# Performance work log

Hardware: AMD Instinct MI355X
Metric: run time of the kernel (lower is better)

The kernel has to match this reference:

```python
import jax, jax.numpy as jnp
import numpy as np


def _gru_step(x, h, W_ih, W_hh, b_ih, b_hh):
    # torch GRUCell math, gate order (r, z, n)
    gx = x @ W_ih.T + b_ih
    gh = h @ W_hh.T + b_hh
    xr, xz, xn = jnp.split(gx, 3, axis=-1)
    hr, hz, hn = jnp.split(gh, 3, axis=-1)
    r = jax.nn.sigmoid(xr + hr)
    z = jax.nn.sigmoid(xz + hz)
    n = jnp.tanh(xn + r * hn)
    return (1.0 - z) * n + z * h


def setup_inputs() -> dict:
    T, B, S, E, H, Dv, EXT = 64, 16, 400, 128, 256, 50000, 50
    key = jax.random.key(0)
    ks = jax.random.split(key, 32)
    def rn(k, shape, s=0.05):
        return jax.random.normal(k, shape, dtype=jnp.float32) * s
    return {
        'embedded_y': rn(ks[0], (T, B, E), 1.0),
        'encode_outputs': rn(ks[1], (S, B, 2 * H), 1.0),
        'init_state': rn(ks[2], (B, H), 1.0),
        'x_mask': jnp.ones((S, B, 1), jnp.float32),
        'y_mask': jnp.ones((T, B, 1), jnp.float32),
        'x_index': jax.random.randint(ks[3], (S, B), 0, Dv + EXT),
        'max_ext_len': EXT,
        'init_coverage': jnp.zeros((B, S), jnp.float32),
        'W_h': rn(ks[4], (2 * H, 2 * H)),
        'W_s': rn(ks[5], (2 * H, H)),
        'W_c': rn(ks[6], (2 * H, 1)),
        'b_attn': rn(ks[7], (2 * H,)),
        'V_attn': rn(ks[8], (1, 2 * H)),
        'gru1_Wih': rn(ks[9], (3 * H, E)),
        'gru1_Whh': rn(ks[10], (3 * H, H)),
        'gru1_bih': rn(ks[11], (3 * H,)),
        'gru1_bhh': rn(ks[12], (3 * H,)),
        'gru2_Wih': rn(ks[13], (3 * H, 2 * H)),
        'gru2_Whh': rn(ks[14], (3 * H, H)),
        'gru2_bih': rn(ks[15], (3 * H,)),
        'gru2_bhh': rn(ks[16], (3 * H,)),
        'V1_w': rn(ks[17], (H, H + 2 * H + E)),
        'V1_b': rn(ks[18], (H,)),
        'V2_w': rn(ks[19], (Dv, H)),
        'V2_b': rn(ks[20], (Dv,)),
        'Wp_w': rn(ks[21], (1, H + 2 * H + E)),
        'Wp_b': rn(ks[22], (1,)),
    }


def reference(embedded_y, encode_outputs, init_state, x_mask, y_mask, x_index,
              max_ext_len, init_coverage, W_h, W_s, W_c, b_attn, V_attn,
              gru1_Wih, gru1_Whh, gru1_bih, gru1_bhh,
              gru2_Wih, gru2_Whh, gru2_bih, gru2_bhh,
              V1_w, V1_b, V2_w, V2_b, Wp_w, Wp_b):
    T, B, E = embedded_y.shape
    S = encode_outputs.shape[0]
    enc_proj = encode_outputs @ W_h.T  # [S,B,2H], time-invariant part of attention

    def step(carry, inp):
        hidden, cov = carry  # [B,H], [B,S]
        y_t, ym_t = inp      # [B,E], [B,1]
        s1 = _gru_step(y_t, hidden, gru1_Wih, gru1_Whh, gru1_bih, gru1_bhh)
        s1 = ym_t * s1 + (1.0 - ym_t) * hidden
        # coverage term: cov.T[:,:,None] is [S,B,1], Linear(1,2H)
        att = enc_proj + s1 @ W_s.T + cov.T[:, :, None] @ W_c.T + b_attn  # [S,B,2H]
        score = (jnp.tanh(att) * x_mask) @ V_attn.T                      # [S,B,1]
        score = jnp.where(x_mask == 0, -1e9, score)
        attn = jax.nn.softmax(score, axis=0)                             # over source len
        ctx = jnp.sum(attn * encode_outputs, axis=0)                     # [B,2H]
        s2 = _gru_step(ctx, s1, gru2_Wih, gru2_Whh, gru2_bih, gru2_bhh)
        s2 = ym_t * s2 + (1.0 - ym_t) * s1
        waw = attn[:, :, 0].T                                            # [B,S]
        return (s2, cov + waw), (s2, ctx, waw, cov)

    (_, _), (hs, cvs, waws, covs) = jax.lax.scan(
        step, (init_state, init_coverage), (embedded_y, y_mask))

    # WordProbLayer (pointer-generator)
    h = jnp.concatenate([hs, cvs, embedded_y], axis=2)         # [T,B,H+2H+E]
    logit = jnp.tanh(h @ V1_w.T + V1_b) @ V2_w.T + V2_b        # [T,B,Dv]
    y_dec = jax.nn.softmax(logit, axis=2)
    y_dec = jnp.concatenate(
        [y_dec, jnp.zeros((T, B, max_ext_len), y_dec.dtype)], axis=2)
    g = jax.nn.sigmoid(h @ Wp_w.T + Wp_b)                      # [T,B,1]
    xids = jnp.broadcast_to(x_index.T[None], (T, B, S))        # [T,B,S]
    ti = jnp.arange(T)[:, None, None]
    bi = jnp.arange(B)[None, :, None]
    y_pred = (g * y_dec).at[ti, bi, xids].add((1.0 - g) * waws)
    return (y_pred, hs, waws, covs)
```

## Files before the change

kernel.cpp:

```cpp
#include <hip/hip_runtime.h>
#include <hip/hip_bf16.h>

typedef unsigned short ushort_t;
typedef unsigned int u32;
typedef _Float16 f16;
typedef __attribute__((ext_vector_type(8))) short short8;
typedef __attribute__((ext_vector_type(4))) float f32x4;
typedef __attribute__((ext_vector_type(8))) _Float16 f16x8;
typedef __attribute__((ext_vector_type(4))) unsigned int u32x4;

#define T_ 64
#define B_ 16
#define S_ 400
#define E_ 128
#define H_ 256
#define H2_ 512
#define DV_ 50000
#define VOC_ 50050
#define CAT_ 896
#define NCLUS 8
#define RSL 50

#define YP_SZ   ((size_t)T_*B_*VOC_)
#define HS_OFF  (YP_SZ)
#define WW_OFF  (HS_OFF + (size_t)T_*B_*H_)
#define CV_OFF  (WW_OFF + (size_t)T_*B_*S_)
#define ENCP16_OFF ((size_t)0)
#define ENC16_OFF  ((size_t)1638400)
#define WS16_OFF   ((size_t)3276800)
#define W216_OFF   ((size_t)3342336)
#define CTXALL_OFF ((size_t)3538944)
#define GX1_OFF    ((size_t)4063232)
#define WH216_OFF  ((size_t)4947968)
#define WH116T_OFF ((size_t)5046272)
#define SYNC_OFF   ((size_t)5144576)
#define S1STR      528
#define S1TAG      520
#define S2STR      816
#define S2TAG      808
#define S2REG      ((size_t)16*NCLUS*S1STR)
#define SYNC_FLOATS ((size_t)16*NCLUS*(S1STR + S2STR))
#define WH16F_OFF  ((size_t)5316608)
#define V1HF_OFF   ((size_t)5447680)

#define WS_ROWSUM 0
#define WS_GV     1024
#define WS_G1     2048

__device__ __forceinline__ float fsig(float x){ return 1.f/(1.f+__expf(-x)); }
__device__ __forceinline__ float ftanh(float x){ float e=__expf(2.f*x); return 1.f - 2.f/(e+1.f); }

#define PADK(k) ((k) + (((k)>>5)<<2))

#define AT_ST(p, v)  __hip_atomic_store((p), (v), __ATOMIC_RELAXED, __HIP_MEMORY_SCOPE_AGENT)
#define AT_LD(p)     __hip_atomic_load((p), __ATOMIC_RELAXED, __HIP_MEMORY_SCOPE_AGENT)
#define AT_STI(p, v) __hip_atomic_store((int*)(p), (v), __ATOMIC_RELAXED, __HIP_MEMORY_SCOPE_AGENT)
#define AT_LDI(p)    __hip_atomic_load((const int*)(p), __ATOMIC_RELAXED, __HIP_MEMORY_SCOPE_AGENT)

#define SM_ENC    0
#define SM_ENCP   51200
#define SM_GH1    102400
#define SM_SWS    105472
#define SM_VP     107776
#define SM_WCP    110080
#define SM_UCTX   112384
#define SM_HID    114432
#define SM_S1     115456
#define SM_G2X    116480
#define SM_G2H    116864
#define SM_COV    117248
#define SM_EV     117504
#define SM_XM     117760
#define SM_YM     118016
#define SM_HIDH   118272
#define SM_S1H    118784
#define SM_CTXH   119296
#define SM_S2S    120320
#define SM_PART   120448
#define SM_B1     120512
#define SM_B2     123584
#define SM_B3     126656
#define SM_GX     129728
#define SM_BYTES  132800

__global__ __launch_bounds__(256)
void cvt16_kernel(const float* src, f16* dst, int n){
  int i = blockIdx.x*256 + threadIdx.x;
  if (i < n) dst[i] = (f16)src[i];
}

__global__ __launch_bounds__(256)
void repack_kernel(const float* enc, f16* enc16){
  int s = blockIdx.x, b = blockIdx.y;
  const float* src = enc + ((size_t)s*B_ + b)*H2_;
  f16* dst = enc16 + ((size_t)b*S_ + s)*H2_;
  for (int k = threadIdx.x; k < H2_; k += 256) dst[k] = (f16)src[k];
}

__global__ __launch_bounds__(256)
void packWhh1_kernel(const float* W, f16* dst){
  int r = blockIdx.x, c = threadIdx.x;
  int jq = c >> 5, cc = c & 31;
  dst[((size_t)jq*768 + r)*32 + cc] = (f16)W[(size_t)r*H_ + c];
}

__global__ __launch_bounds__(256)
void gx1_kernel(const float* emb, const float* Wih1, const float* bih1, float* dout){
  __shared__ float As[64][33];
  __shared__ float Bs[128][33];
  int m0 = blockIdx.x*64, n0 = blockIdx.y*128;
  int tx = threadIdx.x & 15, ty = threadIdx.x >> 4;
  float acc[4][8] = {};
  for (int kt = 0; kt < E_; kt += 32){
    for (int l = threadIdx.x; l < 64*32; l += 256){
      int m = l>>5, k = l&31; As[m][k] = emb[(size_t)(m0+m)*E_ + kt + k];
    }
    for (int l = threadIdx.x; l < 128*32; l += 256){
      int n = l>>5, k = l&31; Bs[n][k] = Wih1[(size_t)(n0+n)*E_ + kt + k];
    }
    __syncthreads();
    for (int k = 0; k < 32; ++k){
      float a[4], bv[8];
      #pragma unroll
      for (int i=0;i<4;++i) a[i] = As[ty+16*i][k];
      #pragma unroll
      for (int j=0;j<8;++j) bv[j] = Bs[tx+16*j][k];
      #pragma unroll
      for (int i=0;i<4;++i)
        #pragma unroll
        for (int j=0;j<8;++j) acc[i][j] += a[i]*bv[j];
    }
    __syncthreads();
  }
  #pragma unroll
  for (int i=0;i<4;++i)
    #pragma unroll
    for (int j=0;j<8;++j){
      int m = m0 + ty + 16*i, n = n0 + tx + 16*j;
      dout[GX1_OFF + (size_t)m*768 + n] = acc[i][j] + bih1[n];
    }
}

__global__ __launch_bounds__(256)
void encproj_mfma(const f16* enc16, const f16* Wh16, const float* battn, f16* ep16){
  int nx = blockIdx.x, my = blockIdx.y, bz = blockIdx.z;
  int tid = threadIdx.x;
  int w = tid >> 6, lane = tid & 63;
  int c16 = lane & 15, kg = lane >> 4;
  int m0 = my*64, n0 = nx*128 + w*32;
  f32x4 acc[4][2] = {};
  int col0 = n0 + c16, col1 = n0 + 16 + c16;
  for (int ks = 0; ks < 16; ++ks){
    int k0 = ks*32 + kg*8;
    f16x8 b0 = *(const f16x8*)(Wh16 + (size_t)col0*H2_ + k0);
    f16x8 b1 = *(const f16x8*)(Wh16 + (size_t)col1*H2_ + k0);
    #pragma unroll
    for (int mf = 0; mf < 4; ++mf){
      int s = m0 + mf*16 + c16; if (s > S_-1) s = S_-1;
      f16x8 a = *(const f16x8*)(enc16 + ((size_t)bz*S_ + s)*H2_ + k0);
      acc[mf][0] = __builtin_amdgcn_mfma_f32_16x16x32_f16(a, b0, acc[mf][0], 0, 0, 0);
      acc[mf][1] = __builtin_amdgcn_mfma_f32_16x16x32_f16(a, b1, acc[mf][1], 0, 0, 0);
    }
  }
  #pragma unroll
  for (int mf = 0; mf < 4; ++mf)
    #pragma unroll
    for (int nf = 0; nf < 2; ++nf){
      int col = n0 + nf*16 + c16;
      float bb = battn[col];
      #pragma unroll
      for (int r = 0; r < 4; ++r){
        int s = m0 + mf*16 + kg*4 + r;
        if (s < S_) ep16[((size_t)bz*S_ + s)*H2_ + col] = (f16)(acc[mf][nf][r] + bb);
      }
    }
}

template<int R, int K, bool PAD>
__device__ __forceinline__ void gemv_f16t(const f16* W, const f16* xh, float* out_l, int tid){
  int o = tid >> 3, l8 = tid & 7;
  constexpr int NI = K/64;
  const f16x8* x8 = (const f16x8*)xh;
  f16x8 xv[NI];
  #pragma unroll
  for (int i = 0; i < NI; ++i) xv[i] = x8[i*8 + l8];
  #pragma unroll
  for (int it = 0; it < R/128; ++it){
    int d = o + it*128;
    const f16x8* w8 = (const f16x8*)(W + (size_t)d*K);
    float acc = 0.f;
    #pragma unroll
    for (int i = 0; i < NI; ++i){
      f16x8 w = w8[i*8 + l8];
      #pragma unroll
      for (int e = 0; e < 8; ++e) acc += (float)w[e] * (float)xv[i][e];
    }
    acc += __shfl_xor(acc,1,8); acc += __shfl_xor(acc,2,8); acc += __shfl_xor(acc,4,8);
    if (l8 == 0) out_l[PAD ? PADK(d) : d] = acc;
  }
}

__device__ __forceinline__ void spin_tags(const float* base, int stride, int tagoff, int want, int tid){
  if (tid < 64){
    bool mine = tid < NCLUS;
    const float* tp = base + (size_t)(mine ? tid : 0)*stride + tagoff;
    while (true){
      int v = mine ? AT_LDI(tp) : want;
      if (__all(v == want)) break;
      __builtin_amdgcn_s_sleep(1);
    }
  }
  __syncthreads();
}

__global__ __launch_bounds__(1024)
void scan_kernel(const float* xm, const float* ym,
                 const float* bhh1, const float* bih2, const float* bhh2,
                 const float* Wc, const float* Vat,
                 const float* inith, const float* initc,
                 float* dout)
{
  extern __shared__ char smem[];
  f16*   enc_s  = (f16*)(smem + SM_ENC);
  f16*   encp_s = (f16*)(smem + SM_ENCP);
  float* gh1_l  = (float*)(smem + SM_GH1);
  float* sWs_p  = (float*)(smem + SM_SWS);
  float* Vp     = (float*)(smem + SM_VP);
  float* Wcp    = (float*)(smem + SM_WCP);
  float* uctx   = (float*)(smem + SM_UCTX);
  float* hid_l  = (float*)(smem + SM_HID);
  float* s1_l   = (float*)(smem + SM_S1);
  float* g2x_l  = (float*)(smem + SM_G2X);
  float* g2h_l  = (float*)(smem + SM_G2H);
  float* cov_l  = (float*)(smem + SM_COV);
  float* ev_l   = (float*)(smem + SM_EV);
  float* xm_l   = (float*)(smem + SM_XM);
  float* ym_l   = (float*)(smem + SM_YM);
  f16*   hidh   = (f16*)(smem + SM_HIDH);
  f16*   s1h    = (f16*)(smem + SM_S1H);
  f16*   ctxh   = (f16*)(smem + SM_CTXH);
  float* s2s    = (float*)(smem + SM_S2S);
  float* part_l = (float*)(smem + SM_PART);
  float* b1l    = (float*)(smem + SM_B1);
  float* b2l    = (float*)(smem + SM_B2);
  float* b3l    = (float*)(smem + SM_B3);
  float* gxbuf  = (float*)(smem + SM_GX);

  const f16* Ws16   = (const f16*)(dout + WS16_OFF);
  const f16* W216   = (const f16*)(dout + W216_OFF);
  const f16* Wh216  = (const f16*)(dout + WH216_OFF);
  const f16* Wh116T = (const f16*)(dout + WH116T_OFF);
  const float* gx1  = dout + GX1_OFF;

  int blk = blockIdx.x, tid = threadIdx.x;
  int b = blk & 15, jj = blk >> 4;
  int wv = tid >> 6, ln = tid & 63;

  float* sl1 = dout + SYNC_OFF + (size_t)b*NCLUS*S1STR;
  float* sl2 = dout + SYNC_OFF + S2REG + (size_t)b*NCLUS*S2STR;
  float* sl1my = sl1 + (size_t)jj*S1STR;
  float* sl2my = sl2 + (size_t)jj*S2STR;

  {
    const u32x4* encg  = (const u32x4*)(dout + ENC16_OFF)  + (size_t)b*25600 + jj*3200;
    const u32x4* encpg = (const u32x4*)(dout + ENCP16_OFF) + (size_t)b*25600 + jj*3200;
    u32x4* encs4  = (u32x4*)enc_s;
    u32x4* encps4 = (u32x4*)encp_s;
    for (int i = tid; i < 3200; i += 1024){ encs4[i] = encg[i]; encps4[i] = encpg[i]; }
  }
  if (tid < 32)  s2s[tid] = inith[b*H_ + jj*32 + tid];
  if (tid < 512){ Vp[PADK(tid)] = Vat[tid]; Wcp[PADK(tid)] = Wc[tid]; }
  if (tid < RSL){ int s = jj*RSL + tid; cov_l[tid] = initc[b*S_ + s]; xm_l[tid] = xm[(size_t)s*B_ + b]; }
  if (tid >= 512 && tid < 576) ym_l[tid-512] = ym[(tid-512)*B_ + b];
  if (tid < 768){ b1l[tid] = bhh1[tid]; b2l[tid] = bih2[tid]; b3l[tid] = bhh2[tid];
                  gxbuf[tid] = gx1[(size_t)b*768 + tid]; }
  __syncthreads();
  if (tid < 768){
    const f16x8* p8 = (const f16x8*)(Wh116T + ((size_t)jj*768 + tid)*32);
    float acc = 0.f;
    #pragma unroll
    for (int c4 = 0; c4 < 4; ++c4){
      f16x8 w = p8[c4];
      #pragma unroll
      for (int e = 0; e < 8; ++e) acc += (float)w[e] * s2s[c4*8+e];
    }
    AT_ST(&sl2my[tid], acc);
  } else if (tid < 800){
    AT_ST(&sl2my[768 + (tid-768)], s2s[tid-768]);
  }
  __syncthreads();
  if (tid == 0) AT_STI(&sl2my[S2TAG], 1);

  for (int t = 0; t < T_; ++t){
    int row = t*B_ + b;
    int want = t + 1;
    spin_tags(sl2, S2STR, S2TAG, want, tid);
    if (tid < 768){
      float a = 0.f;
      #pragma unroll
      for (int q = 0; q < NCLUS; ++q) a += AT_LD(&sl2[(size_t)q*S2STR + tid]);
      gh1_l[tid] = a;
    } else {
      int j = tid - 768;
      float h = AT_LD(&sl2[(size_t)(j>>5)*S2STR + 768 + (j&31)]);
      hid_l[j] = h; hidh[j] = (f16)h;
    }
    __syncthreads();
    if (tid < 256){
      int j = tid;
      float r = fsig(gxbuf[j]      + gh1_l[j]      + b1l[j]);
      float z = fsig(gxbuf[256+j]  + gh1_l[256+j]  + b1l[256+j]);
      float n = ftanh(gxbuf[512+j] + r*(gh1_l[512+j] + b1l[512+j]));
      float h = hid_l[j];
      float ymv = ym_l[t];
      float s1 = ymv*((1.f-z)*n + z*h) + (1.f-ymv)*h;
      s1_l[j] = s1; s1h[j] = (f16)s1;
    }
    __syncthreads();
    gemv_f16t<512,256,true>(Ws16, s1h, sWs_p, tid);
    __syncthreads();
    {
      int kp = PADK(ln*8);
      float4 sA = *(const float4*)&sWs_p[kp], sB = *(const float4*)&sWs_p[kp+4];
      float4 vA = *(const float4*)&Vp[kp],    vB = *(const float4*)&Vp[kp+4];
      float4 cA = *(const float4*)&Wcp[kp],   cB = *(const float4*)&Wcp[kp+4];
      const f16x8* eps = (const f16x8*)encp_s;
      #pragma unroll
      for (int i = 0; i < 4; ++i){
        int r = wv + 16*i;
        if (r < RSL){
          f16x8 eu = eps[r*64 + ln];
          float cv = cov_l[r];
          float sc = 0.f;
          sc += ftanh((float)eu[0] + sA.x + cv*cA.x)*vA.x;
          sc += ftanh((float)eu[1] + sA.y + cv*cA.y)*vA.y;
          sc += ftanh((float)eu[2] + sA.z + cv*cA.z)*vA.z;
          sc += ftanh((float)eu[3] + sA.w + cv*cA.w)*vA.w;
          sc += ftanh((float)eu[4] + sB.x + cv*cB.x)*vB.x;
          sc += ftanh((float)eu[5] + sB.y + cv*cB.y)*vB.y;
          sc += ftanh((float)eu[6] + sB.z + cv*cB.z)*vB.z;
          sc += ftanh((float)eu[7] + sB.w + cv*cB.w)*vB.w;
          sc += __shfl_xor(sc,1);  sc += __shfl_xor(sc,2);  sc += __shfl_xor(sc,4);
          sc += __shfl_xor(sc,8);  sc += __shfl_xor(sc,16); sc += __shfl_xor(sc,32);
          if (ln == 0){
            float xmv = xm_l[r];
            ev_l[r] = __expf((xmv == 0.f) ? -1e9f : xmv*sc);
          }
        }
      }
    }
    __syncthreads();
    if (tid < 512){
      float acc = 0.f;
      #pragma unroll 5
      for (int s = 0; s < RSL; ++s) acc += ev_l[s] * (float)enc_s[s*H2_ + tid];
      AT_ST(&sl1my[tid], acc);
    } else if (tid >= 960){
      int l = tid - 960;
      float v = (l < RSL) ? ev_l[l] : 0.f;
      v += __shfl_xor(v,1);  v += __shfl_xor(v,2);  v += __shfl_xor(v,4);
      v += __shfl_xor(v,8);  v += __shfl_xor(v,16); v += __shfl_xor(v,32);
      if (l == 0) AT_ST(&sl1my[512], v);
    }
    __syncthreads();
    if (tid == 0) AT_STI(&sl1my[S1TAG], want);
    float gxn = 0.f;
    if (tid < 768){
      int tn = (t+1 < T_) ? t+1 : t;
      gxn = gx1[(size_t)(tn*B_ + b)*768 + tid];
    }
    {
      int o = tid >> 3, l8 = tid & 7;
      if (o < 96){
        int g = o >> 5, m = o & 31, wrow = g*256 + jj*32 + m;
        const f16x8* w8 = (const f16x8*)(Wh216 + (size_t)wrow*H_);
        const f16x8* x8 = (const f16x8*)s1h;
        float acc = 0.f;
        #pragma unroll
        for (int i = 0; i < 4; ++i){
          f16x8 w = w8[i*8 + l8], x = x8[i*8 + l8];
          #pragma unroll
          for (int e = 0; e < 8; ++e) acc += (float)w[e] * (float)x[e];
        }
        acc += __shfl_xor(acc,1,8); acc += __shfl_xor(acc,2,8); acc += __shfl_xor(acc,4,8);
        if (l8 == 0) g2h_l[o] = acc;
      }
    }
    if (tid < 768) gxbuf[tid] = gxn;
    spin_tags(sl1, S1STR, S1TAG, want, tid);
    if (tid < 512){
      float us = 0.f;
      #pragma unroll
      for (int q = 0; q < NCLUS; ++q) us += AT_LD(&sl1[(size_t)q*S1STR + tid]);
      uctx[tid] = us;
    } else if (tid < 512 + NCLUS){
      part_l[tid-512] = AT_LD(&sl1[(size_t)(tid-512)*S1STR + 512]);
    }
    __syncthreads();
    {
      float es = 0.f;
      #pragma unroll
      for (int q = 0; q < NCLUS; ++q) es += part_l[q];
      float inv = 1.f/es;
      if (tid < 512){
        float v = uctx[tid]*inv;
        ctxh[tid] = (f16)v;
        if (jj == 0) __builtin_nontemporal_store(v, &dout[CTXALL_OFF + (size_t)row*H2_ + tid]);
      } else if (tid >= 640 && tid < 640 + RSL){
        int r = tid - 640;
        float w_ = ev_l[r]*inv;
        size_t ro = (size_t)row*S_ + jj*RSL + r;
        __builtin_nontemporal_store(w_, &dout[WW_OFF + ro]);
        float co = cov_l[r];
        __builtin_nontemporal_store(co, &dout[CV_OFF + ro]);
        cov_l[r] = co + w_;
      }
    }
    __syncthreads();
    {
      int o = tid >> 3, l8 = tid & 7;
      if (o < 96){
        int g = o >> 5, m = o & 31, wrow = g*256 + jj*32 + m;
        const f16x8* w8 = (const f16x8*)(W216 + (size_t)wrow*H2_);
        const f16x8* x8 = (const f16x8*)ctxh;
        float acc = 0.f;
        #pragma unroll
        for (int i = 0; i < 8; ++i){
          f16x8 w = w8[i*8 + l8], x = x8[i*8 + l8];
          #pragma unroll
          for (int e = 0; e < 8; ++e) acc += (float)w[e] * (float)x[e];
        }
        acc += __shfl_xor(acc,1,8); acc += __shfl_xor(acc,2,8); acc += __shfl_xor(acc,4,8);
        if (l8 == 0) g2x_l[o] = acc;
      }
    }
    __syncthreads();
    if (tid < 32){
      int i = tid, j = jj*32 + i;
      float r = fsig(g2x_l[i]     + b2l[j]     + g2h_l[i]    + b3l[j]);
      float z = fsig(g2x_l[32+i]  + b2l[256+j] + g2h_l[32+i] + b3l[256+j]);
      float n = ftanh(g2x_l[64+i] + b2l[512+j] + r*(g2h_l[64+i] + b3l[512+j]));
      float s1v = s1_l[j];
      float ymv = ym_l[t];
      float s2 = ymv*((1.f-z)*n + z*s1v) + (1.f-ymv)*s1v;
      s2s[i] = s2;
      AT_ST(&sl2my[768 + i], s2);
      __builtin_nontemporal_store(s2, &dout[HS_OFF + (size_t)row*H_ + j]);
    }
    __syncthreads();
    if (tid < 768){
      const f16x8* p8 = (const f16x8*)(Wh116T + ((size_t)jj*768 + tid)*32);
      float acc = 0.f;
      #pragma unroll
      for (int c4 = 0; c4 < 4; ++c4){
        f16x8 w = p8[c4];
        #pragma unroll
        for (int e = 0; e < 8; ++e) acc += (float)w[e] * s2s[c4*8+e];
      }
      AT_ST(&sl2my[tid], acc);
    }
    __syncthreads();
    if (tid == 0) AT_STI(&sl2my[S2TAG], t + 2);
  }
}

__global__ __launch_bounds__(512)
void head_kernel(const float* emb, const f16* V1H, const float* V1b,
                 const float* Wpw, const float* Wpb, float* dout, float* ws)
{
  __shared__ float hc[2][CAT_];
  int t = blockIdx.x, b0 = blockIdx.y*2, tid = threadIdx.x;
  for (int i = tid; i < 2*CAT_; i += 512){
    int bb = i / CAT_, k = i % CAT_;
    int b = b0 + bb;
    float v;
    if (k < H_)           v = dout[HS_OFF     + ((size_t)(t*B_+b))*H_  + k];
    else if (k < H_+H2_)  v = dout[CTXALL_OFF + ((size_t)(t*B_+b))*H2_ + (k-H_)];
    else                  v = emb[((size_t)(t*B_+b))*E_ + (k-H_-H2_)];
    hc[bb][k] = v;
  }
  __syncthreads();
  __hip_bfloat16* G1 = (__hip_bfloat16*)(ws + WS_G1);
  {
    int j = tid & 255, bb = tid >> 8;
    const f16x8* wv8 = (const f16x8*)(V1H + (size_t)j*CAT_);
    float acc = 0.f;
    #pragma unroll 4
    for (int kk = 0; kk < CAT_/8; ++kk){
      f16x8 w = wv8[kk];
      #pragma unroll
      for (int e = 0; e < 8; ++e) acc += hc[bb][kk*8+e]*(float)w[e];
    }
    G1[((size_t)(t*B_ + b0 + bb))*H_ + j] = __float2bfloat16(ftanh(acc + V1b[j]));
  }
  if (tid < 128){
    int bb = tid >> 6, l = tid & 63;
    float acc = 0.f;
    for (int k = l; k < CAT_; k += 64) acc += hc[bb][k]*Wpw[k];
    acc += __shfl_xor(acc,1);  acc += __shfl_xor(acc,2);  acc += __shfl_xor(acc,4);
    acc += __shfl_xor(acc,8);  acc += __shfl_xor(acc,16); acc += __shfl_xor(acc,32);
    if (l == 0) ws[WS_GV + t*B_ + b0 + bb] = fsig(acc + Wpb[0]);
  }
}

__global__ __launch_bounds__(256)
void gemm2_kernel(const ushort_t* G1, const float* V2w, const float* V2b,
                  float* dout, float* rowsum)
{
  __shared__ float rows_l[256];
  int tid = threadIdx.x;
  rows_l[tid] = 0.f;
  int m0 = blockIdx.y * 256;
  int n0 = blockIdx.x * 64;
  int lane = tid & 63, w = tid >> 6;
  int c16 = lane & 15, kg = lane >> 4;
  int col = n0 + w*16 + c16;
  int colc = col < DV_ ? col : DV_-1;
  bool valid = col < DV_;
  f32x4 acc[16] = {};
  const float* brow = V2w + (size_t)colc*H_;
  for (int ks = 0; ks < 8; ++ks){
    int k0 = ks*32 + kg*8;
    short8 bf;
    #pragma unroll
    for (int i = 0; i < 8; ++i){
      __hip_bfloat16 hb = __float2bfloat16(brow[k0+i]);
      union { __hip_bfloat16 h; short s; } u; u.h = hb;
      bf[i] = u.s;
    }
    #pragma unroll
    for (int mf = 0; mf < 16; ++mf){
      const short8* ap = (const short8*)(G1 + ((size_t)(m0 + mf*16 + c16))*H_ + k0);
      acc[mf] = __builtin_amdgcn_mfma_f32_16x16x32_bf16(*ap, bf, acc[mf], 0, 0, 0);
    }
  }
  float bias = valid ? V2b[colc] : 0.f;
  __syncthreads();
  #pragma unroll
  for (int mf = 0; mf < 16; ++mf){
    #pragma unroll
    for (int r = 0; r < 4; ++r){
      float v = valid ? __expf(acc[mf][r] + bias) : 0.f;
      int rloc = mf*16 + kg*4 + r;
      if (valid) __builtin_nontemporal_store(v, &dout[(size_t)(m0 + rloc)*VOC_ + col]);
      float s = v;
      s += __shfl_xor(s, 1, 16); s += __shfl_xor(s, 2, 16);
      s += __shfl_xor(s, 4, 16); s += __shfl_xor(s, 8, 16);
      if (c16 == 0) atomicAdd(&rows_l[rloc], s);
    }
  }
  __syncthreads();
  atomicAdd(&rowsum[m0 + tid], rows_l[tid]);
}

__global__ __launch_bounds__(256)
void normscatter_kernel(float* dout, const float* ws, const int* xidx){
  int row = blockIdx.x; int b = row & 15;
  float gv = ws[WS_GV + row];
  float sc = gv / ws[WS_ROWSUM + row];
  float g1 = 1.f - gv;
  float2* y2 = (float2*)(dout + (size_t)row * VOC_);
  for (int i = threadIdx.x; i < VOC_/2; i += 256){
    float2 v = y2[i];
    int e0 = 2*i;
    v.x = (e0   < DV_) ? v.x*sc : 0.f;
    v.y = (e0+1 < DV_) ? v.y*sc : 0.f;
    y2[i] = v;
  }
  __syncthreads();
  const float* ww = dout + WW_OFF + (size_t)row*S_;
  float* y = dout + (size_t)row*VOC_;
  for (int s = threadIdx.x; s < S_; s += 256){
    atomicAdd(&y[xidx[(size_t)s*B_ + b]], g1*ww[s]);
  }
}

extern "C" void kernel_launch(void* const* d_in, const int* in_sizes, int n_in,
                              void* d_out, int out_size, void* d_ws, size_t ws_size,
                              hipStream_t stream)
{
  (void)in_sizes; (void)n_in; (void)out_size; (void)ws_size;
  const float* emb   = (const float*)d_in[0];
  const float* enc   = (const float*)d_in[1];
  const float* inith = (const float*)d_in[2];
  const float* xmask = (const float*)d_in[3];
  const float* ymask = (const float*)d_in[4];
  const int*   xidx  = (const int*)d_in[5];
  const float* initc = (const float*)d_in[7];
  const float* Wh    = (const float*)d_in[8];
  const float* Wss   = (const float*)d_in[9];
  const float* Wc    = (const float*)d_in[10];
  const float* battn = (const float*)d_in[11];
  const float* Vat   = (const float*)d_in[12];
  const float* Wih1  = (const float*)d_in[13];
  const float* Whh1  = (const float*)d_in[14];
  const float* bih1  = (const float*)d_in[15];
  const float* bhh1  = (const float*)d_in[16];
  const float* Wih2  = (const float*)d_in[17];
  const float* Whh2  = (const float*)d_in[18];
  const float* bih2  = (const float*)d_in[19];
  const float* bhh2  = (const float*)d_in[20];
  const float* V1w   = (const float*)d_in[21];
  const float* V1b   = (const float*)d_in[22];
  const float* V2w   = (const float*)d_in[23];
  const float* V2b   = (const float*)d_in[24];
  const float* Wpw   = (const float*)d_in[25];
  const float* Wpb   = (const float*)d_in[26];
  float* out = (float*)d_out;
  float* ws  = (float*)d_ws;

  hipFuncSetAttribute(reinterpret_cast<const void*>(scan_kernel),
                      hipFuncAttributeMaxDynamicSharedMemorySize, SM_BYTES);

  hipMemsetAsync(d_ws, 0, 2048*sizeof(float), stream);
  hipMemsetAsync(out + SYNC_OFF, 0, SYNC_FLOATS*sizeof(float), stream);
  cvt16_kernel<<<512,  256, 0, stream>>>(Wss,  (f16*)(out + WS16_OFF), H2_*H_);
  cvt16_kernel<<<1536, 256, 0, stream>>>(Wih2, (f16*)(out + W216_OFF), 3*H_*H2_);
  cvt16_kernel<<<768,  256, 0, stream>>>(Whh2, (f16*)(out + WH216_OFF), 3*H_*H_);
  cvt16_kernel<<<1024, 256, 0, stream>>>(Wh,   (f16*)(out + WH16F_OFF), H2_*H2_);
  cvt16_kernel<<<896,  256, 0, stream>>>(V1w,  (f16*)(out + V1HF_OFF), H_*CAT_);
  packWhh1_kernel<<<768, 256, 0, stream>>>(Whh1, (f16*)(out + WH116T_OFF));
  repack_kernel<<<dim3(S_, B_), 256, 0, stream>>>(enc, (f16*)(out + ENC16_OFF));
  gx1_kernel<<<dim3(16, 6), 256, 0, stream>>>(emb, Wih1, bih1, out);
  encproj_mfma<<<dim3(4, 7, B_), 256, 0, stream>>>((const f16*)(out + ENC16_OFF),
      (const f16*)(out + WH16F_OFF), battn, (f16*)(out + ENCP16_OFF));
  scan_kernel<<<128, 1024, SM_BYTES, stream>>>(xmask, ymask,
      bhh1, bih2, bhh2, Wc, Vat, inith, initc, out);
  head_kernel<<<dim3(T_, 8), 512, 0, stream>>>(emb, (const f16*)(out + V1HF_OFF),
      V1b, Wpw, Wpb, out, ws);
  gemm2_kernel<<<dim3(782, 4), 256, 0, stream>>>((const ushort_t*)(ws + WS_G1), V2w, V2b, out, ws + WS_ROWSUM);
  normscatter_kernel<<<1024, 256, 0, stream>>>(out, ws, xidx);
}
```

Baseline: 1.852 ms.

## Merge weight-conversion kernels into one prep launch and trim scan-loop barrier

Replaces seven separate fp32-to-fp16 conversion and repack launches with a single prep kernel that picks its segment from the block index, cutting launch overhead and inter-kernel gaps. Inside the recurrent scan loop, the per-step reduction of context partials now reads the sync slots directly instead of staging them through shared memory, which removes a __syncthreads per step. It also drops an unused fp16 hidden-state copy. The cost is that every thread redundantly reads the eight normaliser partials with atomic loads.

```diff
diff --git a/kernel.cpp b/kernel.cpp
--- a/kernel.cpp
+++ b/kernel.cpp
@@ -84,24 +84,32 @@
 #define SM_BYTES  132800
 
 __global__ __launch_bounds__(256)
-void cvt16_kernel(const float* src, f16* dst, int n){
-  int i = blockIdx.x*256 + threadIdx.x;
-  if (i < n) dst[i] = (f16)src[i];
-}
-
-__global__ __launch_bounds__(256)
-void repack_kernel(const float* enc, f16* enc16){
-  int s = blockIdx.x, b = blockIdx.y;
-  const float* src = enc + ((size_t)s*B_ + b)*H2_;
-  f16* dst = enc16 + ((size_t)b*S_ + s)*H2_;
-  for (int k = threadIdx.x; k < H2_; k += 256) dst[k] = (f16)src[k];
-}
-
-__global__ __launch_bounds__(256)
-void packWhh1_kernel(const float* W, f16* dst){
-  int r = blockIdx.x, c = threadIdx.x;
-  int jq = c >> 5, cc = c & 31;
-  dst[((size_t)jq*768 + r)*32 + cc] = (f16)W[(size_t)r*H_ + c];
+void prep_kernel(const float* Wss, const float* Wih2, const float* Whh2,
+                 const float* Wh, const float* V1w, const float* Whh1,
+                 const float* enc, float* out){
+  int blk = blockIdx.x, tid = threadIdx.x;
+  if (blk < 512){
+    int i = blk*256 + tid; ((f16*)(out + WS16_OFF))[i] = (f16)Wss[i];
+  } else if (blk < 2048){
+    int i = (blk-512)*256 + tid; ((f16*)(out + W216_OFF))[i] = (f16)Wih2[i];
+  } else if (blk < 2816){
+    int i = (blk-2048)*256 + tid; ((f16*)(out + WH216_OFF))[i] = (f16)Whh2[i];
+  } else if (blk < 3840){
+    int i = (blk-2816)*256 + tid; ((f16*)(out + WH16F_OFF))[i] = (f16)Wh[i];
+  } else if (blk < 4736){
+    int i = (blk-3840)*256 + tid; ((f16*)(out + V1HF_OFF))[i] = (f16)V1w[i];
+  } else if (blk < 5504){
+    int r = blk - 4736;
+    int jq = tid >> 5, cc = tid & 31;
+    ((f16*)(out + WH116T_OFF))[((size_t)jq*768 + r)*32 + cc] = (f16)Whh1[(size_t)r*H_ + tid];
+  } else {
+    int idx = blk - 5504;
+    int s = idx % S_, b = idx / S_;
+    const float* src = enc + ((size_t)s*B_ + b)*H2_;
+    f16* dst = (f16*)(out + ENC16_OFF) + ((size_t)b*S_ + s)*H2_;
+    dst[tid] = (f16)src[tid];
+    dst[tid + 256] = (f16)src[tid + 256];
+  }
 }
 
 __global__ __launch_bounds__(256)
@@ -227,7 +235,6 @@
   float* sWs_p  = (float*)(smem + SM_SWS);
   float* Vp     = (float*)(smem + SM_VP);
   float* Wcp    = (float*)(smem + SM_WCP);
-  float* uctx   = (float*)(smem + SM_UCTX);
   float* hid_l  = (float*)(smem + SM_HID);
   float* s1_l   = (float*)(smem + SM_S1);
   float* g2x_l  = (float*)(smem + SM_G2X);
@@ -236,11 +243,9 @@
   float* ev_l   = (float*)(smem + SM_EV);
   float* xm_l   = (float*)(smem + SM_XM);
   float* ym_l   = (float*)(smem + SM_YM);
-  f16*   hidh   = (f16*)(smem + SM_HIDH);
   f16*   s1h    = (f16*)(smem + SM_S1H);
   f16*   ctxh   = (f16*)(smem + SM_CTXH);
   float* s2s    = (float*)(smem + SM_S2S);
-  float* part_l = (float*)(smem + SM_PART);
   float* b1l    = (float*)(smem + SM_B1);
   float* b2l    = (float*)(smem + SM_B2);
   float* b3l    = (float*)(smem + SM_B3);
@@ -302,8 +307,7 @@
       gh1_l[tid] = a;
     } else {
       int j = tid - 768;
-      float h = AT_LD(&sl2[(size_t)(j>>5)*S2STR + 768 + (j&31)]);
-      hid_l[j] = h; hidh[j] = (f16)h;
+      hid_l[j] = AT_LD(&sl2[(size_t)(j>>5)*S2STR + 768 + (j&31)]);
     }
     __syncthreads();
     if (tid < 256){
@@ -388,22 +392,16 @@
     }
     if (tid < 768) gxbuf[tid] = gxn;
     spin_tags(sl1, S1STR, S1TAG, want, tid);
-    if (tid < 512){
-      float us = 0.f;
-      #pragma unroll
-      for (int q = 0; q < NCLUS; ++q) us += AT_LD(&sl1[(size_t)q*S1STR + tid]);
-      uctx[tid] = us;
-    } else if (tid < 512 + NCLUS){
-      part_l[tid-512] = AT_LD(&sl1[(size_t)(tid-512)*S1STR + 512]);
-    }
-    __syncthreads();
     {
       float es = 0.f;
       #pragma unroll
-      for (int q = 0; q < NCLUS; ++q) es += part_l[q];
+      for (int q = 0; q < NCLUS; ++q) es += AT_LD(&sl1[(size_t)q*S1STR + 512]);
       float inv = 1.f/es;
       if (tid < 512){
-        float v = uctx[tid]*inv;
+        float us = 0.f;
+        #pragma unroll
+        for (int q = 0; q < NCLUS; ++q) us += AT_LD(&sl1[(size_t)q*S1STR + tid]);
+        float v = us*inv;
         ctxh[tid] = (f16)v;
         if (jj == 0) __builtin_nontemporal_store(v, &dout[CTXALL_OFF + (size_t)row*H2_ + tid]);
       } else if (tid >= 640 && tid < 640 + RSL){
@@ -614,13 +612,7 @@
 
   hipMemsetAsync(d_ws, 0, 2048*sizeof(float), stream);
   hipMemsetAsync(out + SYNC_OFF, 0, SYNC_FLOATS*sizeof(float), stream);
-  cvt16_kernel<<<512,  256, 0, stream>>>(Wss,  (f16*)(out + WS16_OFF), H2_*H_);
-  cvt16_kernel<<<1536, 256, 0, stream>>>(Wih2, (f16*)(out + W216_OFF), 3*H_*H2_);
-  cvt16_kernel<<<768,  256, 0, stream>>>(Whh2, (f16*)(out + WH216_OFF), 3*H_*H_);
-  cvt16_kernel<<<1024, 256, 0, stream>>>(Wh,   (f16*)(out + WH16F_OFF), H2_*H2_);
-  cvt16_kernel<<<896,  256, 0, stream>>>(V1w,  (f16*)(out + V1HF_OFF), H_*CAT_);
-  packWhh1_kernel<<<768, 256, 0, stream>>>(Whh1, (f16*)(out + WH116T_OFF));
-  repack_kernel<<<dim3(S_, B_), 256, 0, stream>>>(enc, (f16*)(out + ENC16_OFF));
+  prep_kernel<<<11904, 256, 0, stream>>>(Wss, Wih2, Whh2, Wh, V1w, Whh1, enc, out);
   gx1_kernel<<<dim3(16, 6), 256, 0, stream>>>(emb, Wih1, bih1, out);
   encproj_mfma<<<dim3(4, 7, B_), 256, 0, stream>>>((const f16*)(out + ENC16_OFF),
       (const f16*)(out + WH16F_OFF), battn, (f16*)(out + ENCP16_OFF));
```

Result: no change. 1.858 ms (+0.3%).
